# Optimization experiments

Measured on AMD Instinct MI355X. Metric: run time of the kernel, lower is better.

The kernel has to match this reference:

```python
import jax, jax.numpy as jnp
import numpy as np
import math

B, T, H = 16, 2048, 128

def setup_inputs() -> dict:
    key = jax.random.key(0)
    kq, kk, kv = jax.random.split(key, 3)
    q = jax.random.normal(kq, (B, T, H), dtype=jnp.float32)
    k = jax.random.normal(kk, (B, T, H), dtype=jnp.float32)
    v = jax.random.normal(kv, (B, T, H), dtype=jnp.float32)
    # causal mask, shape (1,1,T,T) as in the torch module
    mask = jnp.tril(jnp.ones((T, T), dtype=jnp.int32))[None, None]
    return {"q": q, "k": k, "v": v, "mask": mask}

def reference(q, k, v, mask) -> jnp.ndarray:
    scale = math.sqrt(q.shape[-1])
    # (B,T,T) attention logits
    att = jnp.einsum("btd,bsd->bts", q, k) / scale
    m = mask[0, 0]  # (T,T), broadcasts over batch
    att = jnp.where(m == 0, -jnp.inf, att)
    att = jax.nn.softmax(att, axis=-1)
    # dropout is identity in eval mode (p=0.0)
    return jnp.einsum("bts,bsd->btd", att, v)
```

## Files before the change

kernel.cpp:

```cpp
#include <hip/hip_runtime.h>
#include <hip/hip_bf16.h>

#define TT 2048
#define DD 128
#define NB 16
#define KVB 32
#define NTILE 64
#define TILE_BYTES 8192

typedef __bf16 bf16x8 __attribute__((ext_vector_type(8)));
typedef __bf16 bf16x4 __attribute__((ext_vector_type(4)));
typedef float f32x4 __attribute__((ext_vector_type(4)));
typedef float f32x16 __attribute__((ext_vector_type(16)));

#define GLOAD_LDS16(g, l) __builtin_amdgcn_global_load_lds( \
    (const __attribute__((address_space(1))) void*)(g),     \
    (__attribute__((address_space(3))) void*)(l), 16, 0, 0)

__device__ __forceinline__ float warp16_sum(float v) {
    v += __shfl_xor(v, 1);
    v += __shfl_xor(v, 2);
    v += __shfl_xor(v, 4);
    v += __shfl_xor(v, 8);
    return v;
}
__device__ __forceinline__ float bf2f(unsigned int u16) {
    union { unsigned int i; float f; } x; x.i = u16 << 16; return x.f;
}
__device__ __forceinline__ unsigned int pk2(float lo, float hi) {
    unsigned short a = __builtin_bit_cast(unsigned short, (__bf16)lo);
    unsigned short b = __builtin_bit_cast(unsigned short, (__bf16)hi);
    return (unsigned int)a | ((unsigned int)b << 16);
}
__device__ __forceinline__ bf16x8 frag4(unsigned int a, unsigned int b,
                                        unsigned int c, unsigned int d) {
    uint4 u = make_uint4(a, b, c, d);
    return __builtin_bit_cast(bf16x8, u);
}
__device__ __forceinline__ f32x16 z16() {
    f32x16 v;
    #pragma unroll
    for (int i = 0; i < 16; ++i) v[i] = 0.f;
    return v;
}
__device__ __forceinline__ int ncof(int qb, int C) {
    return (4 * qb + 4 + C - 1) / C;
}

__global__ __launch_bounds__(256) void prepass(
    const float* __restrict__ K, const float* __restrict__ V,
    char* __restrict__ KB, char* __restrict__ VTB)
{
    const int t = blockIdx.x;
    const int b = blockIdx.y;
    const int tid = threadIdx.x;
    char* kdst = KB  + (size_t)(b * NTILE + t) * TILE_BYTES;
    char* vdst = VTB + (size_t)(b * NTILE + t) * TILE_BYTES;
    const float* kp = K + ((size_t)b * TT + t * KVB) * DD;
    const float* vp = V + ((size_t)b * TT + t * KVB) * DD;

    #pragma unroll
    for (int it = 0; it < 2; ++it) {
        int key = it * 16 + (tid >> 4);
        int d0  = (tid & 15) * 8;
        const float4* s = (const float4*)(kp + (size_t)key * DD + d0);
        float4 f0 = s[0], f1 = s[1];
        bf16x8 h;
        h[0]=(__bf16)f0.x; h[1]=(__bf16)f0.y; h[2]=(__bf16)f0.z; h[3]=(__bf16)f0.w;
        h[4]=(__bf16)f1.x; h[5]=(__bf16)f1.y; h[6]=(__bf16)f1.z; h[7]=(__bf16)f1.w;
        *(bf16x8*)(kdst + key * 256 + ((d0 * 2) ^ ((key & 15) << 4))) = h;
    }
    #pragma unroll
    for (int it = 0; it < 2; ++it) {
        int d  = tid & 127;
        int k0 = ((tid >> 7) + it * 2) * 8;
        bf16x8 h;
        #pragma unroll
        for (int j = 0; j < 8; ++j)
            h[j] = (__bf16)vp[(size_t)(k0 + j) * DD + d];
        *(bf16x8*)(vdst + (d >> 2) * 256 +
                   (((d & 3) * 64 + 2 * k0) ^ (((d >> 2) & 15) << 4))) = h;
    }
}

__global__ __launch_bounds__(256, 2) void attn_main(
    const float* __restrict__ Q,
    const char* __restrict__ KB, const char* __restrict__ VTB,
    float* __restrict__ O, char* __restrict__ SLOTS,
    int CHUNK, int SLOTS_PER_B)
{
    __shared__ __align__(16) unsigned short Klds[3][4096];
    __shared__ __align__(16) unsigned short Vs[3][4096];

    const int b  = blockIdx.x;
    const int qb = 15 - blockIdx.y;
    const int ntile = 4 * qb + 4;
    const int nc = ncof(qb, CHUNK);
    if ((int)blockIdx.z >= nc) return;
    const int t0 = (int)(((long)blockIdx.z * ntile) / nc);
    const int t1 = (int)(((long)(blockIdx.z + 1) * ntile) / nc);

    const int tid  = threadIdx.x;
    const int lane = tid & 63;
    const int w    = tid >> 6;
    const int ln   = lane & 31;
    const int hi   = lane >> 5;
    const int qrow0 = qb * 128 + w * 32;
    const int q_abs = qrow0 + ln;

    const float SCALE = 0.08838834764831845f;

    const float* qrow = Q + ((size_t)b * TT + q_abs) * DD + 8 * hi;
    bf16x8 qf[8];
    #pragma unroll
    for (int kc = 0; kc < 8; ++kc) {
        float4 f0 = *(const float4*)(qrow + kc * 16);
        float4 f1 = *(const float4*)(qrow + kc * 16 + 4);
        bf16x8 t;
        t[0]=(__bf16)f0.x; t[1]=(__bf16)f0.y; t[2]=(__bf16)f0.z; t[3]=(__bf16)f0.w;
        t[4]=(__bf16)f1.x; t[5]=(__bf16)f1.y; t[6]=(__bf16)f1.z; t[7]=(__bf16)f1.w;
        qf[kc] = t;
    }

    f32x16 o[4];
    #pragma unroll
    for (int dg = 0; dg < 4; ++dg) o[dg] = z16();
    float lsum = 0.f;

    const char* kbase = KB  + (size_t)b * NTILE * TILE_BYTES;
    const char* vbase = VTB + (size_t)b * NTILE * TILE_BYTES;

    auto STAGE = [&](int t, int buf) {
        const char* ks = kbase + (size_t)t * TILE_BYTES;
        const char* vs = vbase + (size_t)t * TILE_BYTES;
        #pragma unroll
        for (int j = 0; j < 2; ++j) {
            int off = (w + j * 4) * 1024 + lane * 16;
            GLOAD_LDS16(ks + off, (char*)Klds[buf] + off);
            GLOAD_LDS16(vs + off, (char*)Vs[buf]  + off);
        }
    };

    STAGE(t0, 0);
    if (t0 + 1 < t1) STAGE(t0 + 1, 1);

    for (int t = t0; t < t1; ++t) {
        const int kb = t * KVB;
        const int cb = (t - t0) % 3;

        if (t + 1 < t1) {
            asm volatile("s_waitcnt vmcnt(4)" ::: "memory");
        } else {
            asm volatile("s_waitcnt vmcnt(0)" ::: "memory");
        }
        __builtin_amdgcn_s_barrier();
        __builtin_amdgcn_sched_barrier(0);

        if (t + 2 < t1) STAGE(t + 2, (t - t0 + 2) % 3);

        if (kb <= qrow0 + 31) {
            const bool edge = (kb + 31 > qrow0);
            const char* kl = (const char*)Klds[cb];
            const char* vl = (const char*)Vs[cb];

            const int swk = (ln & 15) << 4;
            const char* krow = kl + ln * 256;
            f32x16 a0 = z16(), a1 = z16();
            __builtin_amdgcn_s_setprio(1);
            #pragma unroll
            for (int kc = 0; kc < 8; kc += 2) {
                bf16x8 kf0 = *(const bf16x8*)(krow + ((kc * 32 + 16 * hi) ^ swk));
                bf16x8 kf1 = *(const bf16x8*)(krow + (((kc + 1) * 32 + 16 * hi) ^ swk));
                a0 = __builtin_amdgcn_mfma_f32_32x32x16_bf16(kf0, qf[kc],     a0, 0, 0, 0);
                a1 = __builtin_amdgcn_mfma_f32_32x32x16_bf16(kf1, qf[kc + 1], a1, 0, 0, 0);
            }
            __builtin_amdgcn_s_setprio(0);
            float p[16];
            float ls0 = 0.f, ls1 = 0.f;
            #pragma unroll
            for (int reg = 0; reg < 16; ++reg) {
                int key_abs = kb + (reg & 3) + 8 * (reg >> 2) + 4 * hi;
                float pe = __expf((a0[reg] + a1[reg]) * SCALE);
                if (edge && key_abs > q_abs) pe = 0.f;
                p[reg] = pe;
                if (reg & 1) ls1 += pe; else ls0 += pe;
            }
            lsum += ls0 + ls1;
            unsigned int wd[8], xr[8];
            #pragma unroll
            for (int i = 0; i < 8; ++i) wd[i] = pk2(p[2 * i], p[2 * i + 1]);
            #pragma unroll
            for (int i = 0; i < 8; ++i) xr[i] = __shfl_xor(wd[i], 32);
            bf16x8 pa0 = hi ? frag4(xr[2], xr[3], wd[2], wd[3])
                            : frag4(wd[0], wd[1], xr[0], xr[1]);
            bf16x8 pa1 = hi ? frag4(xr[6], xr[7], wd[6], wd[7])
                            : frag4(wd[4], wd[5], xr[4], xr[5]);
            __builtin_amdgcn_s_setprio(1);
            #pragma unroll
            for (int dg = 0; dg < 4; ++dg) {
                int d = dg * 32 + ln;
                const char* vrow = vl + (d >> 2) * 256;
                int base = (d & 3) * 64;
                int swv = ((d >> 2) & 15) << 4;
                bf16x8 vf0 = *(const bf16x8*)(vrow + ((base + 16 * hi) ^ swv));
                bf16x8 vf1 = *(const bf16x8*)(vrow + ((base + 32 + 16 * hi) ^ swv));
                o[dg] = __builtin_amdgcn_mfma_f32_32x32x16_bf16(pa0, vf0, o[dg], 0, 0, 0);
                o[dg] = __builtin_amdgcn_mfma_f32_32x32x16_bf16(pa1, vf1, o[dg], 0, 0, 0);
            }
            __builtin_amdgcn_s_setprio(0);
        }
    }

    const float ltot = lsum + __shfl_xor(lsum, 32);

    if (nc == 1) {
        const float inv = 1.0f / ltot;
        float* op = O + ((size_t)b * TT + qrow0) * DD;
        #pragma unroll
        for (int reg = 0; reg < 16; ++reg) {
            int qr = (reg & 3) + 8 * (reg >> 2) + 4 * hi;
            float iv = __shfl(inv, qr);
            #pragma unroll
            for (int dg = 0; dg < 4; ++dg)
                op[(size_t)qr * DD + dg * 32 + ln] = o[dg][reg] * iv;
        }
    } else {
        int off = 0;
        for (int q = 0; q < qb; ++q) {
            int c = ncof(q, CHUNK);
            if (c >= 2) off += c;
        }
        char* slot = SLOTS + (size_t)(b * SLOTS_PER_B + off + blockIdx.z) * 33280;
        unsigned short* so = (unsigned short*)slot;
        float* sl = (float*)(slot + 32768);
        #pragma unroll
        for (int reg = 0; reg < 16; ++reg) {
            int row = w * 32 + (reg & 3) + 8 * (reg >> 2) + 4 * hi;
            #pragma unroll
            for (int dg = 0; dg < 4; ++dg)
                so[row * 128 + dg * 32 + ln] =
                    __builtin_bit_cast(unsigned short, (__bf16)o[dg][reg]);
        }
        if (hi == 0) sl[w * 32 + ln] = ltot;
    }
}

__global__ __launch_bounds__(256) void attn_combine(
    const char* __restrict__ SLOTS, float* __restrict__ O,
    int CHUNK, int SLOTS_PER_B)
{
    const int qb = blockIdx.x;
    const int b  = blockIdx.y;
    const int nc = ncof(qb, CHUNK);
    if (nc < 2) return;
    int off = 0;
    for (int q = 0; q < qb; ++q) {
        int c = ncof(q, CHUNK);
        if (c >= 2) off += c;
    }
    const int row  = threadIdx.x >> 1;
    const int half = (threadIdx.x & 1) * 64;
    const char* base = SLOTS + (size_t)(b * SLOTS_PER_B + off) * 33280;

    float l = 0.f;
    for (int c = 0; c < nc; ++c)
        l += *(const float*)(base + (size_t)c * 33280 + 32768 + row * 4);
    float inv = 1.0f / l;

    float* op = O + ((size_t)b * TT + qb * 128 + row) * DD + half;
    #pragma unroll
    for (int g = 0; g < 8; ++g) {
        f32x4 a0 = (f32x4){0.f,0.f,0.f,0.f}, a1 = (f32x4){0.f,0.f,0.f,0.f};
        for (int c = 0; c < nc; ++c) {
            const uint4 u = *(const uint4*)(base + (size_t)c * 33280 + row * 256 + half * 2 + g * 16);
            a0[0] += bf2f(u.x & 0xffffu); a0[1] += bf2f(u.x >> 16);
            a0[2] += bf2f(u.y & 0xffffu); a0[3] += bf2f(u.y >> 16);
            a1[0] += bf2f(u.z & 0xffffu); a1[1] += bf2f(u.z >> 16);
            a1[2] += bf2f(u.w & 0xffffu); a1[3] += bf2f(u.w >> 16);
        }
        float4 r0, r1;
        r0.x=a0[0]*inv; r0.y=a0[1]*inv; r0.z=a0[2]*inv; r0.w=a0[3]*inv;
        r1.x=a1[0]*inv; r1.y=a1[1]*inv; r1.z=a1[2]*inv; r1.w=a1[3]*inv;
        *(float4*)(op + g * 8)     = r0;
        *(float4*)(op + g * 8 + 4) = r1;
    }
}

__global__ __launch_bounds__(256) void attn_fb(
    const float* __restrict__ Q, const float* __restrict__ K,
    const float* __restrict__ V, float* __restrict__ O)
{
    __shared__ __align__(16) unsigned short Klds[2][64 * 128];
    __shared__ __align__(16) unsigned short Vsh[2][128 * 64];
    __shared__ __align__(16) unsigned short Plds[4][16 * 64];

    const int qb = 31 - blockIdx.x;
    const int b  = blockIdx.y;
    const int ntile = qb + 1;
    const int tid  = threadIdx.x;
    const int lane = tid & 63;
    const int w    = tid >> 6;
    const int x    = lane & 15;
    const int hi   = lane >> 4;
    const int qrow0 = qb * 64 + w * 16;

    const float* qp    = Q + ((size_t)b * TT + qrow0) * DD;
    const float* kbase = K + (size_t)b * TT * DD;
    const float* vbase = V + (size_t)b * TT * DD;
    const float SCALE = 0.08838834764831845f;

    const int krow = tid >> 5;
    const int d4   = (tid & 31) * 4;
    const int dd   = tid & 127;
    const int g    = tid >> 7;

    bf16x8 qf[4];
    #pragma unroll
    for (int kc = 0; kc < 4; ++kc) {
        const float4* s0 = (const float4*)(qp + x * DD + kc * 32 + 8 * hi);
        float4 f0 = s0[0], f1 = s0[1];
        bf16x8 t;
        t[0]=(__bf16)f0.x; t[1]=(__bf16)f0.y; t[2]=(__bf16)f0.z; t[3]=(__bf16)f0.w;
        t[4]=(__bf16)f1.x; t[5]=(__bf16)f1.y; t[6]=(__bf16)f1.z; t[7]=(__bf16)f1.w;
        qf[kc] = t;
    }
    f32x4 o[8];
    #pragma unroll
    for (int nt = 0; nt < 8; ++nt) o[nt] = (f32x4){0.f,0.f,0.f,0.f};
    float lsum[4] = {0.f,0.f,0.f,0.f};
    float4 kreg[8];
    float  vreg[32];

    auto LOAD = [&](int t) {
        const float* kp = kbase + (size_t)(t * 64) * DD;
        const float* vp = vbase + (size_t)(t * 64) * DD;
        #pragma unroll
        for (int it = 0; it < 8; ++it)
            kreg[it] = *(const float4*)(kp + (size_t)(it * 8 + krow) * DD + d4);
        #pragma unroll
        for (int j = 0; j < 32; ++j)
            vreg[j] = vp[(size_t)(g * 32 + j) * DD + dd];
    };
    auto WRITE = [&](int buf) {
        char* kb8 = (char*)Klds[buf];
        #pragma unroll
        for (int it = 0; it < 8; ++it) {
            int key = it * 8 + krow;
            float4 f = kreg[it];
            bf16x4 h;
            h[0]=(__bf16)f.x; h[1]=(__bf16)f.y; h[2]=(__bf16)f.z; h[3]=(__bf16)f.w;
            *(bf16x4*)(kb8 + key * 256 + ((d4 * 2) ^ ((key & 7) << 4))) = h;
        }
        char* vb8 = (char*)Vsh[buf];
        #pragma unroll
        for (int m4 = 0; m4 < 4; ++m4) {
            bf16x8 h;
            #pragma unroll
            for (int j = 0; j < 8; ++j) h[j] = (__bf16)vreg[m4 * 8 + j];
            *(bf16x8*)(vb8 + dd * 128 + ((g * 64 + m4 * 16) ^ ((dd & 7) << 4))) = h;
        }
    };

    LOAD(0); WRITE(0);
    int cur = 0;
    char* pmine = (char*)Plds[w];

    for (int t = 0; t < ntile; ++t) {
        const int kb = t * 64;
        __syncthreads();
        if (t + 1 < ntile) LOAD(t + 1);

        const bool diag  = (t == qb);
        const int  ntmax = diag ? w : 3;
        const char* kb8  = (const char*)Klds[cur];
        float p[4][4];
        #pragma unroll
        for (int nt = 0; nt < 4; ++nt) {
            int key = nt * 16 + x;
            if (nt <= ntmax) {
                f32x4 acc = (f32x4){0.f,0.f,0.f,0.f};
                #pragma unroll
                for (int kc = 0; kc < 4; ++kc) {
                    int off = key * 256 + ((kc * 64 + 16 * hi) ^ ((key & 7) << 4));
                    bf16x8 bfr = *(const bf16x8*)(kb8 + off);
                    acc = __builtin_amdgcn_mfma_f32_16x16x32_bf16(qf[kc], bfr, acc, 0, 0, 0);
                }
                #pragma unroll
                for (int r = 0; r < 4; ++r) {
                    bool msk = diag && (kb + key > qrow0 + 4 * hi + r);
                    float pe = msk ? 0.f : __expf(acc[r] * SCALE);
                    p[nt][r] = pe;
                    lsum[r] += pe;
                }
            } else {
                #pragma unroll
                for (int r = 0; r < 4; ++r) p[nt][r] = 0.f;
            }
        }
        #pragma unroll
        for (int nt = 0; nt < 4; ++nt)
            #pragma unroll
            for (int r = 0; r < 4; ++r) {
                int q = 4 * hi + r;
                *(unsigned short*)(pmine + q * 128 + (((nt * 16 + x) * 2) ^ ((q & 7) << 4))) =
                    __builtin_bit_cast(unsigned short, (__bf16)p[nt][r]);
            }
        const char* vb8 = (const char*)Vsh[cur];
        #pragma unroll
        for (int kc = 0; kc < 2; ++kc) {
            bf16x8 af = *(const bf16x8*)(pmine + x * 128 + ((kc * 64 + 16 * hi) ^ ((x & 7) << 4)));
            #pragma unroll
            for (int nt = 0; nt < 8; ++nt) {
                int d = nt * 16 + x;
                bf16x8 bfr = *(const bf16x8*)(vb8 + d * 128 + ((kc * 64 + 16 * hi) ^ ((d & 7) << 4)));
                o[nt] = __builtin_amdgcn_mfma_f32_16x16x32_bf16(af, bfr, o[nt], 0, 0, 0);
            }
        }
        if (t + 1 < ntile) WRITE(cur ^ 1);
        cur ^= 1;
    }
    float* op = O + ((size_t)b * TT + qrow0) * DD;
    #pragma unroll
    for (int r = 0; r < 4; ++r) {
        float lr = warp16_sum(lsum[r]);
        float inv = 1.0f / lr;
        #pragma unroll
        for (int nt = 0; nt < 8; ++nt)
            op[(size_t)(4 * hi + r) * DD + nt * 16 + x] = o[nt][r] * inv;
    }
}

extern "C" void kernel_launch(void* const* d_in, const int* in_sizes, int n_in,
                              void* d_out, int out_size, void* d_ws, size_t ws_size,
                              hipStream_t stream) {
    const float* q = (const float*)d_in[0];
    const float* k = (const float*)d_in[1];
    const float* v = (const float*)d_in[2];
    float* out = (float*)d_out;

    const size_t PRE = (size_t)2 * NB * NTILE * TILE_BYTES;
    auto slotsPerB = [](int C) {
        int s = 0;
        for (int qb = 0; qb < 16; ++qb) {
            int nc = (4 * qb + 4 + C - 1) / C;
            if (nc >= 2) s += nc;
        }
        return s;
    };

    char* kb  = (char*)d_ws;
    char* vtb = kb + (size_t)NB * NTILE * TILE_BYTES;
    char* slots = vtb + (size_t)NB * NTILE * TILE_BYTES;

    const int spb12 = slotsPerB(12);
    const int spb16 = slotsPerB(16);

    if (ws_size >= PRE + (size_t)NB * spb12 * 33280) {
        prepass<<<dim3(NTILE, NB), 256, 0, stream>>>(k, v, kb, vtb);
        attn_main<<<dim3(NB, 16, 6), 256, 0, stream>>>(q, kb, vtb, out, slots, 12, spb12);
        attn_combine<<<dim3(16, NB), 256, 0, stream>>>(slots, out, 12, spb12);
    } else if (ws_size >= PRE + (size_t)NB * spb16 * 33280) {
        prepass<<<dim3(NTILE, NB), 256, 0, stream>>>(k, v, kb, vtb);
        attn_main<<<dim3(NB, 16, 4), 256, 0, stream>>>(q, kb, vtb, out, slots, 16, spb16);
        attn_combine<<<dim3(16, NB), 256, 0, stream>>>(slots, out, 16, spb16);
    } else if (ws_size >= PRE) {
        prepass<<<dim3(NTILE, NB), 256, 0, stream>>>(k, v, kb, vtb);
        attn_main<<<dim3(NB, 16, 1), 256, 0, stream>>>(q, kb, vtb, out, slots, 64, 0);
    } else {
        attn_fb<<<dim3(32, NB), 256, 0, stream>>>(q, k, v, out);
    }
}
```

Before: 85.64 us.

## Fuse split-K combine into main kernel via atomic last-block reduction

Drops the separate combine kernel. Each split block now writes its partial output, bumps a per-(batch, q-block) atomic counter, and the last block to arrive does the reduction and writes the final output. The softmax scale times log2(e) is folded into Q during the bf16 conversion, so the inner loop uses a bare exp2 instead of a multiply plus expf. A new tier with chunk size 8 and 8 z-splits is added for finer work splitting, and it needs a memset of the counters plus more slot storage.

```diff
diff --git a/kernel.cpp b/kernel.cpp
--- a/kernel.cpp
+++ b/kernel.cpp
@@ -86,11 +86,12 @@
 __global__ __launch_bounds__(256, 2) void attn_main(
     const float* __restrict__ Q,
     const char* __restrict__ KB, const char* __restrict__ VTB,
-    float* __restrict__ O, char* __restrict__ SLOTS,
+    float* __restrict__ O, char* __restrict__ SLOTS, int* __restrict__ CNT,
     int CHUNK, int SLOTS_PER_B)
 {
     __shared__ __align__(16) unsigned short Klds[3][4096];
     __shared__ __align__(16) unsigned short Vs[3][4096];
+    __shared__ int last_flag;
 
     const int b  = blockIdx.x;
     const int qb = 15 - blockIdx.y;
@@ -108,7 +109,7 @@
     const int qrow0 = qb * 128 + w * 32;
     const int q_abs = qrow0 + ln;
 
-    const float SCALE = 0.08838834764831845f;
+    const float QSCALE = 0.12751744485f;
 
     const float* qrow = Q + ((size_t)b * TT + q_abs) * DD + 8 * hi;
     bf16x8 qf[8];
@@ -117,8 +118,10 @@
         float4 f0 = *(const float4*)(qrow + kc * 16);
         float4 f1 = *(const float4*)(qrow + kc * 16 + 4);
         bf16x8 t;
-        t[0]=(__bf16)f0.x; t[1]=(__bf16)f0.y; t[2]=(__bf16)f0.z; t[3]=(__bf16)f0.w;
-        t[4]=(__bf16)f1.x; t[5]=(__bf16)f1.y; t[6]=(__bf16)f1.z; t[7]=(__bf16)f1.w;
+        t[0]=(__bf16)(f0.x*QSCALE); t[1]=(__bf16)(f0.y*QSCALE);
+        t[2]=(__bf16)(f0.z*QSCALE); t[3]=(__bf16)(f0.w*QSCALE);
+        t[4]=(__bf16)(f1.x*QSCALE); t[5]=(__bf16)(f1.y*QSCALE);
+        t[6]=(__bf16)(f1.z*QSCALE); t[7]=(__bf16)(f1.w*QSCALE);
         qf[kc] = t;
     }
 
@@ -180,7 +183,7 @@
             #pragma unroll
             for (int reg = 0; reg < 16; ++reg) {
                 int key_abs = kb + (reg & 3) + 8 * (reg >> 2) + 4 * hi;
-                float pe = __expf((a0[reg] + a1[reg]) * SCALE);
+                float pe = __builtin_amdgcn_exp2f(a0[reg] + a1[reg]);
                 if (edge && key_abs > q_abs) pe = 0.f;
                 p[reg] = pe;
                 if (reg & 1) ls1 += pe; else ls0 += pe;
@@ -224,13 +227,16 @@
             for (int dg = 0; dg < 4; ++dg)
                 op[(size_t)qr * DD + dg * 32 + ln] = o[dg][reg] * iv;
         }
-    } else {
-        int off = 0;
-        for (int q = 0; q < qb; ++q) {
-            int c = ncof(q, CHUNK);
-            if (c >= 2) off += c;
-        }
-        char* slot = SLOTS + (size_t)(b * SLOTS_PER_B + off + blockIdx.z) * 33280;
+        return;
+    }
+
+    int soff = 0;
+    for (int q = 0; q < qb; ++q) {
+        int c = ncof(q, CHUNK);
+        if (c >= 2) soff += c;
+    }
+    {
+        char* slot = SLOTS + (size_t)(b * SLOTS_PER_B + soff + blockIdx.z) * 33280;
         unsigned short* so = (unsigned short*)slot;
         float* sl = (float*)(slot + 32768);
         #pragma unroll
@@ -243,24 +249,20 @@
         }
         if (hi == 0) sl[w * 32 + ln] = ltot;
     }
-}
-
-__global__ __launch_bounds__(256) void attn_combine(
-    const char* __restrict__ SLOTS, float* __restrict__ O,
-    int CHUNK, int SLOTS_PER_B)
-{
-    const int qb = blockIdx.x;
-    const int b  = blockIdx.y;
-    const int nc = ncof(qb, CHUNK);
-    if (nc < 2) return;
-    int off = 0;
-    for (int q = 0; q < qb; ++q) {
-        int c = ncof(q, CHUNK);
-        if (c >= 2) off += c;
-    }
-    const int row  = threadIdx.x >> 1;
-    const int half = (threadIdx.x & 1) * 64;
-    const char* base = SLOTS + (size_t)(b * SLOTS_PER_B + off) * 33280;
+
+    __syncthreads();
+    if (tid == 0) {
+        __threadfence();
+        int prev = atomicAdd(&CNT[b * 16 + qb], 1);
+        last_flag = (prev == nc - 1);
+    }
+    __syncthreads();
+    if (!last_flag) return;
+    __threadfence();
+
+    const char* base = SLOTS + (size_t)(b * SLOTS_PER_B + soff) * 33280;
+    const int row  = tid >> 1;
+    const int half = (tid & 1) * 64;
 
     float l = 0.f;
     for (int c = 0; c < nc; ++c)
@@ -452,20 +454,27 @@
     char* vtb = kb + (size_t)NB * NTILE * TILE_BYTES;
     char* slots = vtb + (size_t)NB * NTILE * TILE_BYTES;
 
+    const int spb8  = slotsPerB(8);
     const int spb12 = slotsPerB(12);
     const int spb16 = slotsPerB(16);
 
-    if (ws_size >= PRE + (size_t)NB * spb12 * 33280) {
+    auto launchTier = [&](int CHUNK, int spb, int zmax) {
+        int* cnt = (int*)(slots + (size_t)NB * spb * 33280);
+        hipMemsetAsync(cnt, 0, NB * 16 * sizeof(int), stream);
         prepass<<<dim3(NTILE, NB), 256, 0, stream>>>(k, v, kb, vtb);
-        attn_main<<<dim3(NB, 16, 6), 256, 0, stream>>>(q, kb, vtb, out, slots, 12, spb12);
-        attn_combine<<<dim3(16, NB), 256, 0, stream>>>(slots, out, 12, spb12);
-    } else if (ws_size >= PRE + (size_t)NB * spb16 * 33280) {
-        prepass<<<dim3(NTILE, NB), 256, 0, stream>>>(k, v, kb, vtb);
-        attn_main<<<dim3(NB, 16, 4), 256, 0, stream>>>(q, kb, vtb, out, slots, 16, spb16);
-        attn_combine<<<dim3(16, NB), 256, 0, stream>>>(slots, out, 16, spb16);
+        attn_main<<<dim3(NB, 16, zmax), 256, 0, stream>>>(q, kb, vtb, out, slots, cnt, CHUNK, spb);
+    };
+
+    const size_t CNTB = NB * 16 * sizeof(int);
+    if (ws_size >= PRE + (size_t)NB * spb8 * 33280 + CNTB) {
+        launchTier(8, spb8, 8);
+    } else if (ws_size >= PRE + (size_t)NB * spb12 * 33280 + CNTB) {
+        launchTier(12, spb12, 6);
+    } else if (ws_size >= PRE + (size_t)NB * spb16 * 33280 + CNTB) {
+        launchTier(16, spb16, 4);
     } else if (ws_size >= PRE) {
         prepass<<<dim3(NTILE, NB), 256, 0, stream>>>(k, v, kb, vtb);
-        attn_main<<<dim3(NB, 16, 1), 256, 0, stream>>>(q, kb, vtb, out, slots, 64, 0);
+        attn_main<<<dim3(NB, 16, 1), 256, 0, stream>>>(q, kb, vtb, out, slots, nullptr, 64, 0);
     } else {
         attn_fb<<<dim3(32, NB), 256, 0, stream>>>(q, k, v, out);
     }
```

Result: slower. 153.6 us (+79.3%).

## Prescale Q by log2e/sqrt(d) in prepass, use exp2, add chunk-8 split tier

Applied to the files above, without the earlier changes.

The prepass now also converts Q to bf16 and premultiplies it by log2(e)/sqrt(d), storing it in a fragment-ready layout. The main kernel then loads the Q fragments directly and uses a hardware exp2 in place of __expf with a scale multiply. A new chunk-8 split tier is tried first when workspace allows, giving more split-K blocks at the cost of more partial slots for the combine kernel. The extra Q workspace raises the minimum workspace needed for the non-fallback paths, and it also adds a global write and read of Q.

```diff
diff --git a/kernel.cpp b/kernel.cpp
--- a/kernel.cpp
+++ b/kernel.cpp
@@ -47,9 +47,12 @@
     return (4 * qb + 4 + C - 1) / C;
 }
 
+#define QSCALE 0.12751744485f
+
 __global__ __launch_bounds__(256) void prepass(
     const float* __restrict__ K, const float* __restrict__ V,
-    char* __restrict__ KB, char* __restrict__ VTB)
+    const float* __restrict__ Q,
+    char* __restrict__ KB, char* __restrict__ VTB, char* __restrict__ QF)
 {
     const int t = blockIdx.x;
     const int b = blockIdx.y;
@@ -81,10 +84,34 @@
         *(bf16x8*)(vdst + (d >> 2) * 256 +
                    (((d & 3) * 64 + 2 * k0) ^ (((d >> 2) & 15) << 4))) = h;
     }
+    {
+        const int row = t * 32 + (tid >> 3);
+        const int kc  = tid & 7;
+        const int qb  = row >> 7;
+        const int w   = (row >> 5) & 3;
+        const int ln  = row & 31;
+        const float* qp = Q + ((size_t)b * TT + row) * DD + kc * 16;
+        float4 f0 = *(const float4*)(qp);
+        float4 f1 = *(const float4*)(qp + 4);
+        float4 f2 = *(const float4*)(qp + 8);
+        float4 f3 = *(const float4*)(qp + 12);
+        bf16x8 h0, h1;
+        h0[0]=(__bf16)(f0.x*QSCALE); h0[1]=(__bf16)(f0.y*QSCALE);
+        h0[2]=(__bf16)(f0.z*QSCALE); h0[3]=(__bf16)(f0.w*QSCALE);
+        h0[4]=(__bf16)(f1.x*QSCALE); h0[5]=(__bf16)(f1.y*QSCALE);
+        h0[6]=(__bf16)(f1.z*QSCALE); h0[7]=(__bf16)(f1.w*QSCALE);
+        h1[0]=(__bf16)(f2.x*QSCALE); h1[1]=(__bf16)(f2.y*QSCALE);
+        h1[2]=(__bf16)(f2.z*QSCALE); h1[3]=(__bf16)(f2.w*QSCALE);
+        h1[4]=(__bf16)(f3.x*QSCALE); h1[5]=(__bf16)(f3.y*QSCALE);
+        h1[6]=(__bf16)(f3.z*QSCALE); h1[7]=(__bf16)(f3.w*QSCALE);
+        size_t base = ((((size_t)(b * 16 + qb) * 4 + w) * 8 + kc) * 2) * 512 + ln * 16;
+        *(bf16x8*)(QF + base)       = h0;
+        *(bf16x8*)(QF + base + 512) = h1;
+    }
 }
 
 __global__ __launch_bounds__(256, 2) void attn_main(
-    const float* __restrict__ Q,
+    const char* __restrict__ QF,
     const char* __restrict__ KB, const char* __restrict__ VTB,
     float* __restrict__ O, char* __restrict__ SLOTS,
     int CHUNK, int SLOTS_PER_B)
@@ -108,19 +135,11 @@
     const int qrow0 = qb * 128 + w * 32;
     const int q_abs = qrow0 + ln;
 
-    const float SCALE = 0.08838834764831845f;
-
-    const float* qrow = Q + ((size_t)b * TT + q_abs) * DD + 8 * hi;
+    const char* qfb = QF + (((size_t)(b * 16 + qb) * 4 + w) * 16 + hi) * 512 + ln * 16;
     bf16x8 qf[8];
     #pragma unroll
-    for (int kc = 0; kc < 8; ++kc) {
-        float4 f0 = *(const float4*)(qrow + kc * 16);
-        float4 f1 = *(const float4*)(qrow + kc * 16 + 4);
-        bf16x8 t;
-        t[0]=(__bf16)f0.x; t[1]=(__bf16)f0.y; t[2]=(__bf16)f0.z; t[3]=(__bf16)f0.w;
-        t[4]=(__bf16)f1.x; t[5]=(__bf16)f1.y; t[6]=(__bf16)f1.z; t[7]=(__bf16)f1.w;
-        qf[kc] = t;
-    }
+    for (int kc = 0; kc < 8; ++kc)
+        qf[kc] = *(const bf16x8*)(qfb + kc * 1024);
 
     f32x16 o[4];
     #pragma unroll
@@ -180,7 +199,7 @@
             #pragma unroll
             for (int reg = 0; reg < 16; ++reg) {
                 int key_abs = kb + (reg & 3) + 8 * (reg >> 2) + 4 * hi;
-                float pe = __expf((a0[reg] + a1[reg]) * SCALE);
+                float pe = __builtin_amdgcn_exp2f(a0[reg] + a1[reg]);
                 if (edge && key_abs > q_abs) pe = 0.f;
                 p[reg] = pe;
                 if (reg & 1) ls1 += pe; else ls0 += pe;
@@ -225,12 +244,12 @@
                 op[(size_t)qr * DD + dg * 32 + ln] = o[dg][reg] * iv;
         }
     } else {
-        int off = 0;
+        int soff = 0;
         for (int q = 0; q < qb; ++q) {
             int c = ncof(q, CHUNK);
-            if (c >= 2) off += c;
-        }
-        char* slot = SLOTS + (size_t)(b * SLOTS_PER_B + off + blockIdx.z) * 33280;
+            if (c >= 2) soff += c;
+        }
+        char* slot = SLOTS + (size_t)(b * SLOTS_PER_B + soff + blockIdx.z) * 33280;
         unsigned short* so = (unsigned short*)slot;
         float* sl = (float*)(slot + 32768);
         #pragma unroll
@@ -438,7 +457,9 @@
     const float* v = (const float*)d_in[2];
     float* out = (float*)d_out;
 
-    const size_t PRE = (size_t)2 * NB * NTILE * TILE_BYTES;
+    const size_t KVBYTES = (size_t)NB * NTILE * TILE_BYTES;
+    const size_t QFBYTES = (size_t)NB * TT * DD * 2;
+    const size_t PRE = 2 * KVBYTES + QFBYTES;
     auto slotsPerB = [](int C) {
         int s = 0;
         for (int qb = 0; qb < 16; ++qb) {
@@ -448,24 +469,30 @@
         return s;
     };
 
-    char* kb  = (char*)d_ws;
-    char* vtb = kb + (size_t)NB * NTILE * TILE_BYTES;
-    char* slots = vtb + (size_t)NB * NTILE * TILE_BYTES;
-
+    char* kb    = (char*)d_ws;
+    char* vtb   = kb + KVBYTES;
+    char* qf    = vtb + KVBYTES;
+    char* slots = qf + QFBYTES;
+
+    const int spb8  = slotsPerB(8);
     const int spb12 = slotsPerB(12);
     const int spb16 = slotsPerB(16);
 
-    if (ws_size >= PRE + (size_t)NB * spb12 * 33280) {
-        prepass<<<dim3(NTILE, NB), 256, 0, stream>>>(k, v, kb, vtb);
-        attn_main<<<dim3(NB, 16, 6), 256, 0, stream>>>(q, kb, vtb, out, slots, 12, spb12);
-        attn_combine<<<dim3(16, NB), 256, 0, stream>>>(slots, out, 12, spb12);
+    auto launchTier = [&](int CHUNK, int spb, int zmax) {
+        prepass<<<dim3(NTILE, NB), 256, 0, stream>>>(k, v, q, kb, vtb, qf);
+        attn_main<<<dim3(NB, 16, zmax), 256, 0, stream>>>(qf, kb, vtb, out, slots, CHUNK, spb);
+        attn_combine<<<dim3(16, NB), 256, 0, stream>>>(slots, out, CHUNK, spb);
+    };
+
+    if (ws_size >= PRE + (size_t)NB * spb8 * 33280) {
+        launchTier(8, spb8, 8);
+    } else if (ws_size >= PRE + (size_t)NB * spb12 * 33280) {
+        launchTier(12, spb12, 6);
     } else if (ws_size >= PRE + (size_t)NB * spb16 * 33280) {
-        prepass<<<dim3(NTILE, NB), 256, 0, stream>>>(k, v, kb, vtb);
-        attn_main<<<dim3(NB, 16, 4), 256, 0, stream>>>(q, kb, vtb, out, slots, 16, spb16);
-        attn_combine<<<dim3(16, NB), 256, 0, stream>>>(slots, out, 16, spb16);
+        launchTier(16, spb16, 4);
     } else if (ws_size >= PRE) {
-        prepass<<<dim3(NTILE, NB), 256, 0, stream>>>(k, v, kb, vtb);
-        attn_main<<<dim3(NB, 16, 1), 256, 0, stream>>>(q, kb, vtb, out, slots, 64, 0);
+        prepass<<<dim3(NTILE, NB), 256, 0, stream>>>(k, v, q, kb, vtb, qf);
+        attn_main<<<dim3(NB, 16, 1), 256, 0, stream>>>(qf, kb, vtb, out, slots, 64, 0);
     } else {
         attn_fb<<<dim3(32, NB), 256, 0, stream>>>(q, k, v, out);
     }
```

Result: slower. 99.01 us (+15.6%).
